# Kernel tuning notes

Hardware: AMD Instinct MI355X
Metric: run time of the kernel (lower is better)

## Reference

```python
import jax, jax.numpy as jnp
import numpy as np

N = 40000   # query points
M = 40000   # support points
H = 32      # neighbors per query
CIN = 64
COUT = 64
KS = 3      # kernel points per dim
PDIM = 3
K = KS ** PDIM  # 27 kernel points
RADIUS = 1.0
KP_EXTENT = RADIUS / (KS - 1) * PDIM ** 0.5


def _kernel_points():
    # replicates KPConv.getKernelPoints: grid of KS^PDIM points in a ball of RADIUS
    xyz = np.linspace(-1.0, 1.0, KS)
    pts = np.meshgrid(*PDIM * [xyz])
    pts = np.vstack([p.flatten() for p in pts]).T  # [K, PDIM]
    pts = pts / PDIM ** 0.5
    return (pts * RADIUS).astype(np.float32)


def setup_inputs() -> dict:
    key = jax.random.key(0)
    k1, k2, k3, k4, k5 = jax.random.split(key, 5)
    q_pts = jax.random.uniform(k1, (N, PDIM), dtype=jnp.float32) * 10.0
    s_pts = jax.random.uniform(k2, (M, PDIM), dtype=jnp.float32) * 10.0
    neighb_inds = jax.random.randint(k3, (N, H), 0, M + 1)  # M == shadow index
    x = jax.random.normal(k4, (M, CIN), dtype=jnp.float32)
    # kaiming-uniform-like init for weights [K, CIN, COUT]
    bound = (6.0 / ((1.0 + 5.0) * CIN)) ** 0.5
    weights = jax.random.uniform(k5, (K, CIN, COUT), dtype=jnp.float32,
                                 minval=-bound, maxval=bound)
    kernel_points = jnp.asarray(_kernel_points())
    return {"q_pts": q_pts, "s_pts": s_pts, "neighb_inds": neighb_inds,
            "x": x, "weights": weights, "kernel_points": kernel_points}


def reference(q_pts, s_pts, neighb_inds, x, weights, kernel_points):
    # append shadow support point (far away) and zero shadow feature
    s_pts_p = jnp.concatenate(
        [s_pts, jnp.full((1, s_pts.shape[-1]), 1e6, dtype=s_pts.dtype)], axis=0)
    x_p = jnp.concatenate(
        [x, jnp.zeros((1, x.shape[-1]), dtype=x.dtype)], axis=0)

    neighbors = s_pts_p[neighb_inds] - q_pts[:, None, :]        # [N, H, 3]
    neighb_x = x_p[neighb_inds]                                  # [N, H, CIN]

    # distance of each neighbor to each kernel point
    diff = neighbors[:, :, None, :] - kernel_points              # [N, H, K, 3]
    sq_d = jnp.sum(diff * diff, axis=-1)                         # [N, H, K]
    all_w = jnp.clip(1.0 - jnp.sqrt(sq_d) / KP_EXTENT, 0.0)      # [N, H, K]

    # all_weights^T @ neighb_x  -> [N, K, CIN]
    weighted = jnp.einsum('nhk,nhc->nkc', all_w, neighb_x)
    # per-kernel-point matmul with weights [K, CIN, COUT], summed over K
    out = jnp.einsum('nkc,kco->no', weighted, weights)           # [N, COUT]
    return out
```

## Files before the change

### kernel.cpp

```cpp
#include <hip/hip_runtime.h>

typedef short bf16x8 __attribute__((ext_vector_type(8)));
typedef float f32x4  __attribute__((ext_vector_type(4)));

#define HN    32
#define CIN   64
#define KP    27
#define QB    64
#define CAPB  96
#define NTB   1024
#define OSTR  65

#define QB2   32
#define CAP2  64
#define OSTR2 68

#define INV_EXT 1.1547005383792517f
#define CUT2    3.4821f

__device__ __forceinline__ unsigned f2bf(float f){
    union{float fv;unsigned u;}v; v.fv=f;
    unsigned u=v.u;
    u += 0x7fffu + ((u>>16)&1u);
    return u>>16;
}

__global__ void pack_spts(const float* __restrict__ s, float4* __restrict__ o, int M){
    int i = blockIdx.x*256 + threadIdx.x;
    if (i < M) o[i] = make_float4(s[i*3+0], s[i*3+1], s[i*3+2], 0.f);
}

__global__ void pack_wt2(const float* __restrict__ W, unsigned short* __restrict__ Wt2){
    int tid = blockIdx.x*256 + threadIdx.x;
    if (tid >= KP*8*64) return;
    int lane = tid & 63;
    int f  = (tid>>6) & 7;
    int k  = tid >> 9;
    int ot = f>>1, ks = f&1, g = lane>>4;
    unsigned r[8];
#pragma unroll
    for (int j=0;j<8;++j)
        r[j] = f2bf(W[(size_t)k*4096 + (size_t)(ks*32 + g*8 + j)*64 + ot*16 + (lane&15)]);
    uint4 v; v.x=r[0]|(r[1]<<16); v.y=r[2]|(r[3]<<16); v.z=r[4]|(r[5]<<16); v.w=r[6]|(r[7]<<16);
    *(uint4*)&Wt2[(size_t)tid*8] = v;
}

__global__ __launch_bounds__(256)
void kp_prep2(const float* __restrict__ s, const float* __restrict__ W,
              float4* __restrict__ o, unsigned short* __restrict__ Wt2, int M)
{
    int tid = blockIdx.x*256 + threadIdx.x;
    if (tid < M) o[tid] = make_float4(s[tid*3+0], s[tid*3+1], s[tid*3+2], 0.f);
    if (tid < KP*8*64){
        int lane = tid & 63;
        int f  = (tid>>6) & 7;
        int kk = tid >> 9;
        int ot = f>>1, ks = f&1, gg = lane>>4;
        unsigned r[8];
#pragma unroll
        for (int j=0;j<8;++j)
            r[j] = f2bf(W[(size_t)kk*4096 + (size_t)(ks*32 + gg*8 + j)*64 + ot*16 + (lane&15)]);
        uint4 v; v.x=r[0]|(r[1]<<16); v.y=r[2]|(r[3]<<16); v.z=r[4]|(r[5]<<16); v.w=r[6]|(r[7]<<16);
        *(uint4*)&Wt2[(size_t)tid*8] = v;
    }
}

__device__ __forceinline__ void loadB(const unsigned short* __restrict__ Wt2, int k, int lane,
                                      bf16x8 (&b)[8]){
    const unsigned short* base = Wt2 + ((size_t)(k*8)*64 + lane)*8;
#pragma unroll
    for (int f=0;f<8;++f) b[f] = *(const bf16x8*)(base + f*512);
}
__device__ __forceinline__ bf16x8 ldBf(const unsigned short* __restrict__ Wt2, int k, int f, int lane){
    return *(const bf16x8*)(Wt2 + ((size_t)(k*8 + f)*64 + lane)*8);
}
__device__ __forceinline__ void loadB_w(const float* __restrict__ W, int k, int lane, int g,
                                        bf16x8 (&b)[8]){
#pragma unroll
    for (int f=0;f<8;++f){
        int ot=f>>1, ks=f&1;
        union{unsigned u[4]; bf16x8 v;} bb;
#pragma unroll
        for (int jj=0;jj<4;++jj){
            unsigned l0=f2bf(W[(size_t)k*4096 + (size_t)(ks*32+g*8+2*jj)*64   + ot*16+(lane&15)]);
            unsigned l1=f2bf(W[(size_t)k*4096 + (size_t)(ks*32+g*8+2*jj+1)*64 + ot*16+(lane&15)]);
            bb.u[jj]=l0|(l1<<16);
        }
        b[f]=bb.v;
    }
}

__global__ __launch_bounds__(256,5)
void kpconv_fused(const float* __restrict__ q_pts, const int* __restrict__ inds,
                  const float* __restrict__ x, const float* __restrict__ kpts,
                  const float4* __restrict__ sp4, const unsigned short* __restrict__ Wt2,
                  float* __restrict__ out, int N, int M)
{
    __shared__ unsigned short rows[64*CIN];
    __shared__ __align__(16) float wlds[KP*64];
    __shared__ __align__(16) float outacc[QB2*OSTR2];
    __shared__ float qls[QB2*3];
    __shared__ float bx[CAP2], by[CAP2], bz[CAP2];
    __shared__ __align__(16) int bq[CAP2];
    __shared__ int bixs[CAP2];
    __shared__ int cnt;

    const int t    = threadIdx.x;
    const int lane = t & 63;
    const int wv   = t >> 6;
    const int g    = lane >> 4;
    const int r15  = lane & 15;
    const int nq0  = blockIdx.x * QB2;
    const int NP   = N*HN;

    for (int j=t; j<QB2*OSTR2; j+=256) outacc[j]=0.f;
    for (int j=t; j<QB2*3;    j+=256){ int gi=nq0*3+j; qls[j]=(gi<N*3)? q_pts[gi]:0.f; }
    if (t < CAP2) bq[t]=0;
    if (t==0) cnt=0;
    __syncthreads();

#pragma unroll
    for (int jj=0; jj<4; ++jj){
        int pl   = jj*256 + t;
        int pair = nq0*HN + pl;
        if (pair < NP){
            int idx = inds[pair];
            if ((unsigned)idx < (unsigned)M){
                int q = pl >> 5;
                float4 s4 = sp4[idx];
                float px=s4.x-qls[q*3], py=s4.y-qls[q*3+1], pz=s4.z-qls[q*3+2];
                if (px*px+py*py+pz*pz <= CUT2){
                    int sl = atomicAdd(&cnt, 1);
                    if (sl < CAP2){ bx[sl]=px; by[sl]=py; bz[sl]=pz; bq[sl]=q; bixs[sl]=idx; }
                }
            }
        }
    }
    __syncthreads();
    const int total = cnt;

    auto processTile = [&](int cc){
        const int nrow = (cc + 15) & ~15;
        const int f0 = wv*2, f1 = wv*2+1;
        bf16x8 Bc0 = ldBf(Wt2, 0, f0, lane);
        bf16x8 Bc1 = ldBf(Wt2, 0, f1, lane);
        for (int it=t; it<nrow*8; it+=256){
            int rl=it>>3, c8=it&7;
            uint4 v; v.x=0u; v.y=0u; v.z=0u; v.w=0u;
            if (rl < cc){
                int ix = bixs[rl];
                const float4* xr = (const float4*)(x + (size_t)ix*CIN);
                float4 fr0=xr[c8*2], fr1=xr[c8*2+1];
                v.x=f2bf(fr0.x)|(f2bf(fr0.y)<<16); v.y=f2bf(fr0.z)|(f2bf(fr0.w)<<16);
                v.z=f2bf(fr1.x)|(f2bf(fr1.y)<<16); v.w=f2bf(fr1.z)|(f2bf(fr1.w)<<16);
            }
            int ba = rl*128 + ((c8*16)^((rl&7)<<4));
            *(uint4*)((char*)rows+ba) = v;
        }
        for (int i=t; i<KP*64; i+=256){
            int row = i&63;
            if (row >= nrow) continue;
            int k = i>>6;
            float w=0.f;
            if (row < cc){
                float dx=bx[row]-kpts[k*3+0];
                float dy=by[row]-kpts[k*3+1];
                float dz=bz[row]-kpts[k*3+2];
                w = fmaxf(1.f - sqrtf(dx*dx+dy*dy+dz*dz)*INV_EXT, 0.f);
            }
            wlds[i]=w;
        }
        __syncthreads();

        const char* rb = (const char*)rows;
        bf16x8 A0[4], A1[4];
#pragma unroll
        for (int rt=0; rt<4; ++rt){
            if (rt*16 >= cc) continue;
            int row = rt*16 + r15;
            A0[rt] = *(const bf16x8*)(rb + row*128 + (( g*16)    ^((row&7)<<4)));
            A1[rt] = *(const bf16x8*)(rb + row*128 + ((64+g*16)  ^((row&7)<<4)));
        }
        f32x4 acc[4];
#pragma unroll
        for (int rt=0; rt<4; ++rt){ acc[rt][0]=0.f; acc[rt][1]=0.f; acc[rt][2]=0.f; acc[rt][3]=0.f; }

#pragma unroll 1
        for (int k=0; k<KP; ++k){
            int kn = (k+1 < KP) ? (k+1) : k;
            bf16x8 Bn0 = ldBf(Wt2, kn, f0, lane);
            bf16x8 Bn1 = ldBf(Wt2, kn, f1, lane);
            const float* wk = &wlds[k*64];
#pragma unroll
            for (int rt=0; rt<4; ++rt){
                if (rt*16 >= cc) continue;
                f32x4 w4 = *(const f32x4*)(wk + rt*16 + g*4);
                bool act = (w4[0]>0.f)|(w4[1]>0.f)|(w4[2]>0.f)|(w4[3]>0.f);
                if (__any(act)){
                    f32x4 c; c[0]=0.f; c[1]=0.f; c[2]=0.f; c[3]=0.f;
                    c = __builtin_amdgcn_mfma_f32_16x16x32_bf16(A0[rt], Bc0, c, 0,0,0);
                    c = __builtin_amdgcn_mfma_f32_16x16x32_bf16(A1[rt], Bc1, c, 0,0,0);
                    acc[rt][0] += w4[0]*c[0];
                    acc[rt][1] += w4[1]*c[1];
                    acc[rt][2] += w4[2]*c[2];
                    acc[rt][3] += w4[3]*c[3];
                }
            }
            Bc0 = Bn0; Bc1 = Bn1;
        }
#pragma unroll
        for (int rt=0; rt<4; ++rt){
            if (rt*16 >= cc) continue;
            int4 q4 = *(const int4*)&bq[rt*16 + g*4];
#pragma unroll
            for (int rr=0; rr<4; ++rr){
                float val = acc[rt][rr];
                int qv = (rr==0)? q4.x : (rr==1)? q4.y : (rr==2)? q4.z : q4.w;
                if (val != 0.f)
                    atomicAdd(&outacc[qv*OSTR2 + wv*16 + r15], val);
            }
        }
        __syncthreads();
    };

    if (total <= CAP2){
        if (total > 0) processTile(total);
    } else {
        for (int w=0; w<(QB2*HN)/64; ++w){
            __syncthreads();
            if (t==0) cnt=0;
            __syncthreads();
            if (t < 64){
                int pl = w*64 + t, pair = nq0*HN + pl;
                if (pair < NP){
                    int idx = inds[pair];
                    if ((unsigned)idx < (unsigned)M){
                        int q = pl >> 5;
                        float4 s4 = sp4[idx];
                        float px=s4.x-qls[q*3], py=s4.y-qls[q*3+1], pz=s4.z-qls[q*3+2];
                        if (px*px+py*py+pz*pz <= CUT2){
                            int sl = atomicAdd(&cnt, 1);
                            bx[sl]=px; by[sl]=py; bz[sl]=pz; bq[sl]=q; bixs[sl]=idx;
                        }
                    }
                }
            }
            __syncthreads();
            if (cnt > 0) processTile(cnt);
        }
    }
    __syncthreads();

    for (int j=t; j<QB2*16; j+=256){
        int q=j>>4, o4=j&15, n=nq0+q;
        if (n < N)
            ((float4*)out)[(size_t)n*16 + o4] = *(const float4*)&outacc[q*OSTR2 + o4*4];
    }
}


__global__ __launch_bounds__(NTB)
void kpconv6(const float* __restrict__ q_pts, const float* __restrict__ s_pts,
             const int* __restrict__ inds, const float* __restrict__ x,
             const float* __restrict__ W, const float* __restrict__ kpts,
             const float4* __restrict__ sp4, const unsigned short* __restrict__ Wt2,
             int use_ws, float* __restrict__ out, int N, int M)
{
    __shared__ float qls[QB*3];
    __shared__ float posx[CAPB], posy[CAPB], posz[CAPB];
    __shared__ int   eqb[CAPB], eidxb[CAPB];
    __shared__ unsigned short rows[CAPB*CIN];
    __shared__ float outacc[QB*OSTR];
    __shared__ int   cnt;

    const int t    = threadIdx.x;
    const int lane = t & 63;
    const int wv   = t >> 6;
    const int g    = lane >> 4;
    const int r15  = lane & 15;
    const int nq0  = blockIdx.x * QB;

    const int k0 = wv, k1 = wv + 16;
    const bool has2 = (k1 < KP);

    bf16x8 B0[8], B1[8];
    if (use_ws){
        loadB(Wt2, k0, lane, B0);
        loadB(Wt2, has2 ? k1 : k0, lane, B1);
    } else {
        loadB_w(W, k0, lane, g, B0);
        loadB_w(W, has2 ? k1 : k0, lane, g, B1);
    }
    const float k0x=kpts[k0*3+0], k0y=kpts[k0*3+1], k0z=kpts[k0*3+2];
    float k1x=0.f,k1y=0.f,k1z=0.f;
    if (has2){ k1x=kpts[k1*3+0]; k1y=kpts[k1*3+1]; k1z=kpts[k1*3+2]; }

    for (int j=t; j<QB*OSTR; j+=NTB) outacc[j]=0.f;
    for (int j=t; j<QB*3;   j+=NTB){ int gi=nq0*3+j; qls[j]=(gi<N*3)? q_pts[gi]:0.f; }
    if (t==0) cnt=0;
    __syncthreads();

    auto process = [&](int cc){
        if (cc<=0) return;
        const int ntile=(cc+15)>>4, nrow=ntile*16;
        for (int j=cc+t; j<nrow; j+=NTB){ posx[j]=1e9f; posy[j]=1e9f; posz[j]=1e9f; eqb[j]=0; }
        for (int it=t; it<nrow*8; it+=NTB){
            int e=it>>3, c8=it&7;
            uint4 v; v.x=0u; v.y=0u; v.z=0u; v.w=0u;
            if (e<cc){
                const float4* xr=(const float4*)(x+(size_t)eidxb[e]*CIN);
                float4 f0=xr[c8*2], f1=xr[c8*2+1];
                v.x=f2bf(f0.x)|(f2bf(f0.y)<<16); v.y=f2bf(f0.z)|(f2bf(f0.w)<<16);
                v.z=f2bf(f1.x)|(f2bf(f1.y)<<16); v.w=f2bf(f1.z)|(f2bf(f1.w)<<16);
            }
            int ba=e*128+((c8*16)^((e&7)<<4));
            *(uint4*)((char*)rows+ba)=v;
        }
        __syncthreads();
        for (int tile=0; tile<ntile; ++tile){
            const char* rb=(const char*)rows;
            int row=tile*16+r15;
            bf16x8 a0=*(const bf16x8*)(rb+row*128+((g*16)    ^((row&7)<<4)));
            bf16x8 a1=*(const bf16x8*)(rb+row*128+((64+g*16) ^((row&7)<<4)));
            int rbase=tile*16+g*4;
            float w0[4], w1[4]; int qq[4];
#pragma unroll
            for (int r=0;r<4;++r){
                float sx=posx[rbase+r], sy=posy[rbase+r], sz=posz[rbase+r];
                qq[r]=eqb[rbase+r];
                float dx=sx-k0x, dy=sy-k0y, dz=sz-k0z;
                w0[r]=fmaxf(1.f-sqrtf(dx*dx+dy*dy+dz*dz)*INV_EXT,0.f);
                float ex=sx-k1x, ey=sy-k1y, ez=sz-k1z;
                float w1r=fmaxf(1.f-sqrtf(ex*ex+ey*ey+ez*ez)*INV_EXT,0.f);
                w1[r]=has2? w1r : 0.f;
            }
#pragma unroll
            for (int ot=0;ot<4;++ot){
                f32x4 c={0.f,0.f,0.f,0.f};
                c=__builtin_amdgcn_mfma_f32_16x16x32_bf16(a0,B0[2*ot],c,0,0,0);
                c=__builtin_amdgcn_mfma_f32_16x16x32_bf16(a1,B0[2*ot+1],c,0,0,0);
                f32x4 d={0.f,0.f,0.f,0.f};
                if (has2){
                    d=__builtin_amdgcn_mfma_f32_16x16x32_bf16(a0,B1[2*ot],d,0,0,0);
                    d=__builtin_amdgcn_mfma_f32_16x16x32_bf16(a1,B1[2*ot+1],d,0,0,0);
                }
#pragma unroll
                for (int r=0;r<4;++r){
                    float val=w0[r]*c[r]+w1[r]*d[r];
                    if (val!=0.f) atomicAdd(&outacc[qq[r]*OSTR+ot*16+r15], val);
                }
            }
        }
        __syncthreads();
    };

    for (int it=t; it<QB*HN; it+=NTB){
        int q=it>>5, h=it&31, n=nq0+q;
        bool inr=false; int idx=0; float px=0.f,py=0.f,pz=0.f;
        if (n<N){
            idx=inds[(size_t)n*HN+h];
            if ((unsigned)idx<(unsigned)M){
                float sx,sy,sz;
                if (use_ws){ float4 s4=sp4[idx]; sx=s4.x; sy=s4.y; sz=s4.z; }
                else { sx=s_pts[idx*3]; sy=s_pts[idx*3+1]; sz=s_pts[idx*3+2]; }
                px=sx-qls[q*3]; py=sy-qls[q*3+1]; pz=sz-qls[q*3+2];
                inr=(px*px+py*py+pz*pz)<=CUT2;
            }
        }
        if (inr){
            int sl=atomicAdd(&cnt,1);
            if (sl<CAPB){ eqb[sl]=q; eidxb[sl]=idx; posx[sl]=px; posy[sl]=py; posz[sl]=pz; }
        }
    }
    __syncthreads();
    const int total=cnt;

    if (total<=CAPB){
        process(total);
    } else {
        for (int w=0; w<(QB*HN)/64; ++w){
            __syncthreads();
            if (t==0) cnt=0;
            __syncthreads();
            if (t<64){
                int pair=w*64+t;
                int q=pair>>5, h=pair&31, n=nq0+q;
                if (n<N){
                    int idx=inds[(size_t)n*HN+h];
                    if ((unsigned)idx<(unsigned)M){
                        float sx,sy,sz;
                        if (use_ws){ float4 s4=sp4[idx]; sx=s4.x; sy=s4.y; sz=s4.z; }
                        else { sx=s_pts[idx*3]; sy=s_pts[idx*3+1]; sz=s_pts[idx*3+2]; }
                        float px=sx-qls[q*3], py=sy-qls[q*3+1], pz=sz-qls[q*3+2];
                        if (px*px+py*py+pz*pz<=CUT2){
                            int sl=atomicAdd(&cnt,1);
                            eqb[sl]=q; eidxb[sl]=idx; posx[sl]=px; posy[sl]=py; posz[sl]=pz;
                        }
                    }
                }
            }
            __syncthreads();
            process(cnt);
        }
    }
    __syncthreads();

    for (int j=t; j<QB*CIN; j+=NTB){
        int q=j>>6, o=j&63, n=nq0+q;
        if (n<N) out[(size_t)n*CIN+o]=outacc[q*OSTR+o];
    }
}

extern "C" void kernel_launch(void* const* d_in, const int* in_sizes, int n_in,
                              void* d_out, int out_size, void* d_ws, size_t ws_size,
                              hipStream_t stream)
{
    const float* q_pts=(const float*)d_in[0];
    const float* s_pts=(const float*)d_in[1];
    const int*   inds =(const int*)d_in[2];
    const float* x    =(const float*)d_in[3];
    const float* W    =(const float*)d_in[4];
    const float* kpts =(const float*)d_in[5];
    float* outp=(float*)d_out;
    int N=in_sizes[0]/3;
    int M=in_sizes[1]/3;

    char* wsb=(char*)d_ws;
    float4* sp4=(float4*)wsb;
    unsigned short* Wt2=(unsigned short*)(wsb + (size_t)M*16);

    const size_t WT2B = (size_t)KP*8*64*8*2;
    size_t need = (size_t)M*16 + WT2B;

    if (ws_size >= need){
        int prepN = (M > KP*8*64) ? M : KP*8*64;
        hipLaunchKernelGGL(kp_prep2, dim3((prepN+255)/256), dim3(256), 0, stream,
                           s_pts, W, sp4, Wt2, M);
        int nblocks = (N + QB2 - 1) / QB2;
        hipLaunchKernelGGL(kpconv_fused, dim3(nblocks), dim3(256), 0, stream,
                           q_pts, inds, x, kpts, sp4, Wt2, outp, N, M);
        return;
    }

    hipLaunchKernelGGL(kpconv6, dim3((N+QB-1)/QB), dim3(NTB), 0, stream,
                       q_pts, s_pts, inds, x, W, kpts, sp4, Wt2, 0, outp, N, M);
}
```

Measured before the change: 41.34 us.

## Split kernel points across waves instead of output tiles in fused KPConv

The fused kernel changes its work split. Before, each wave owned one 16-column output tile and looped over all 27 kernel points. Now each wave owns a strided subset of kernel points, loads all 8 B fragments per kernel point, and computes all four output tiles over 32-row chunks. The neighbor index and support-point loads are batched ahead of the filtering, and the feature-row gathers are issued before the weight computation so their latency overlaps. Launch bounds drop occupancy from 5 to 4 blocks per CU to make room for the larger accumulator and B register sets. This also raises atomic traffic into shared-memory outacc, because each wave now contributes partial sums for every output column. Dead pack kernels and the use_ws path in the fallback kernel are removed.

New measurement: 51.43 us. 1.24x slower.

```diff
diff --git a/kernel.cpp b/kernel.cpp
--- a/kernel.cpp
+++ b/kernel.cpp
@@ -23,26 +23,6 @@
     unsigned u=v.u;
     u += 0x7fffu + ((u>>16)&1u);
     return u>>16;
-}
-
-__global__ void pack_spts(const float* __restrict__ s, float4* __restrict__ o, int M){
-    int i = blockIdx.x*256 + threadIdx.x;
-    if (i < M) o[i] = make_float4(s[i*3+0], s[i*3+1], s[i*3+2], 0.f);
-}
-
-__global__ void pack_wt2(const float* __restrict__ W, unsigned short* __restrict__ Wt2){
-    int tid = blockIdx.x*256 + threadIdx.x;
-    if (tid >= KP*8*64) return;
-    int lane = tid & 63;
-    int f  = (tid>>6) & 7;
-    int k  = tid >> 9;
-    int ot = f>>1, ks = f&1, g = lane>>4;
-    unsigned r[8];
-#pragma unroll
-    for (int j=0;j<8;++j)
-        r[j] = f2bf(W[(size_t)k*4096 + (size_t)(ks*32 + g*8 + j)*64 + ot*16 + (lane&15)]);
-    uint4 v; v.x=r[0]|(r[1]<<16); v.y=r[2]|(r[3]<<16); v.z=r[4]|(r[5]<<16); v.w=r[6]|(r[7]<<16);
-    *(uint4*)&Wt2[(size_t)tid*8] = v;
 }
 
 __global__ __launch_bounds__(256)
@@ -71,9 +51,6 @@
 #pragma unroll
     for (int f=0;f<8;++f) b[f] = *(const bf16x8*)(base + f*512);
 }
-__device__ __forceinline__ bf16x8 ldBf(const unsigned short* __restrict__ Wt2, int k, int f, int lane){
-    return *(const bf16x8*)(Wt2 + ((size_t)(k*8 + f)*64 + lane)*8);
-}
 __device__ __forceinline__ void loadB_w(const float* __restrict__ W, int k, int lane, int g,
                                         bf16x8 (&b)[8]){
 #pragma unroll
@@ -90,7 +67,7 @@
     }
 }
 
-__global__ __launch_bounds__(256,5)
+__global__ __launch_bounds__(256,4)
 void kpconv_fused(const float* __restrict__ q_pts, const int* __restrict__ inds,
                   const float* __restrict__ x, const float* __restrict__ kpts,
                   const float4* __restrict__ sp4, const unsigned short* __restrict__ Wt2,
@@ -101,8 +78,7 @@
     __shared__ __align__(16) float outacc[QB2*OSTR2];
     __shared__ float qls[QB2*3];
     __shared__ float bx[CAP2], by[CAP2], bz[CAP2];
-    __shared__ __align__(16) int bq[CAP2];
-    __shared__ int bixs[CAP2];
+    __shared__ int bq[CAP2], bixs[CAP2];
     __shared__ int cnt;
 
     const int t    = threadIdx.x;
@@ -119,44 +95,44 @@
     if (t==0) cnt=0;
     __syncthreads();
 
+    int idxv[4];
 #pragma unroll
     for (int jj=0; jj<4; ++jj){
-        int pl   = jj*256 + t;
-        int pair = nq0*HN + pl;
-        if (pair < NP){
-            int idx = inds[pair];
-            if ((unsigned)idx < (unsigned)M){
-                int q = pl >> 5;
-                float4 s4 = sp4[idx];
-                float px=s4.x-qls[q*3], py=s4.y-qls[q*3+1], pz=s4.z-qls[q*3+2];
-                if (px*px+py*py+pz*pz <= CUT2){
-                    int sl = atomicAdd(&cnt, 1);
-                    if (sl < CAP2){ bx[sl]=px; by[sl]=py; bz[sl]=pz; bq[sl]=q; bixs[sl]=idx; }
-                }
+        int pair = nq0*HN + jj*256 + t;
+        idxv[jj] = (pair < NP) ? inds[pair] : M;
+    }
+    float4 s4v[4];
+#pragma unroll
+    for (int jj=0; jj<4; ++jj){
+        int ic = (idxv[jj] < M) ? idxv[jj] : 0;
+        s4v[jj] = sp4[ic];
+    }
+#pragma unroll
+    for (int jj=0; jj<4; ++jj){
+        if (idxv[jj] < M){
+            int q = (jj*256 + t) >> 5;
+            float px=s4v[jj].x-qls[q*3], py=s4v[jj].y-qls[q*3+1], pz=s4v[jj].z-qls[q*3+2];
+            if (px*px+py*py+pz*pz <= CUT2){
+                int sl = atomicAdd(&cnt, 1);
+                if (sl < CAP2){ bx[sl]=px; by[sl]=py; bz[sl]=pz; bq[sl]=q; bixs[sl]=idxv[jj]; }
             }
         }
     }
     __syncthreads();
     const int total = cnt;
 
-    auto processTile = [&](int cc){
+    auto process = [&](int cc){
         const int nrow = (cc + 15) & ~15;
-        const int f0 = wv*2, f1 = wv*2+1;
-        bf16x8 Bc0 = ldBf(Wt2, 0, f0, lane);
-        bf16x8 Bc1 = ldBf(Wt2, 0, f1, lane);
-        for (int it=t; it<nrow*8; it+=256){
-            int rl=it>>3, c8=it&7;
-            uint4 v; v.x=0u; v.y=0u; v.z=0u; v.w=0u;
-            if (rl < cc){
-                int ix = bixs[rl];
-                const float4* xr = (const float4*)(x + (size_t)ix*CIN);
-                float4 fr0=xr[c8*2], fr1=xr[c8*2+1];
-                v.x=f2bf(fr0.x)|(f2bf(fr0.y)<<16); v.y=f2bf(fr0.z)|(f2bf(fr0.w)<<16);
-                v.z=f2bf(fr1.x)|(f2bf(fr1.y)<<16); v.w=f2bf(fr1.z)|(f2bf(fr1.w)<<16);
-            }
-            int ba = rl*128 + ((c8*16)^((rl&7)<<4));
-            *(uint4*)((char*)rows+ba) = v;
-        }
+        int itA=t, itB=t+256;
+        int rlA=itA>>3, c8A=itA&7, rlB=itB>>3, c8B=itB&7;
+        bool vA=(rlA<cc), vB=(rlB<cc);
+        bool wrA=(rlA<nrow), wrB=(rlB<nrow);
+        int ixA = vA ? bixs[rlA] : bixs[0];
+        int ixB = vB ? bixs[rlB] : bixs[0];
+        const float4* xrA = (const float4*)(x + (size_t)ixA*CIN);
+        const float4* xrB = (const float4*)(x + (size_t)ixB*CIN);
+        float4 fA0=xrA[c8A*2], fA1=xrA[c8A*2+1];
+        float4 fB0=xrB[c8B*2], fB1=xrB[c8B*2+1];
         for (int i=t; i<KP*64; i+=256){
             int row = i&63;
             if (row >= nrow) continue;
@@ -170,61 +146,97 @@
             }
             wlds[i]=w;
         }
+        if (wrA){
+            uint4 v; v.x=0u; v.y=0u; v.z=0u; v.w=0u;
+            if (vA){
+                v.x=f2bf(fA0.x)|(f2bf(fA0.y)<<16); v.y=f2bf(fA0.z)|(f2bf(fA0.w)<<16);
+                v.z=f2bf(fA1.x)|(f2bf(fA1.y)<<16); v.w=f2bf(fA1.z)|(f2bf(fA1.w)<<16);
+            }
+            *(uint4*)((char*)rows + rlA*128 + ((c8A*16)^((rlA&7)<<4))) = v;
+        }
+        if (wrB){
+            uint4 v; v.x=0u; v.y=0u; v.z=0u; v.w=0u;
+            if (vB){
+                v.x=f2bf(fB0.x)|(f2bf(fB0.y)<<16); v.y=f2bf(fB0.z)|(f2bf(fB0.w)<<16);
+                v.z=f2bf(fB1.x)|(f2bf(fB1.y)<<16); v.w=f2bf(fB1.z)|(f2bf(fB1.w)<<16);
+            }
+            *(uint4*)((char*)rows + rlB*128 + ((c8B*16)^((rlB&7)<<4))) = v;
+        }
         __syncthreads();
 
         const char* rb = (const char*)rows;
-        bf16x8 A0[4], A1[4];
-#pragma unroll
-        for (int rt=0; rt<4; ++rt){
-            if (rt*16 >= cc) continue;
-            int row = rt*16 + r15;
-            A0[rt] = *(const bf16x8*)(rb + row*128 + (( g*16)    ^((row&7)<<4)));
-            A1[rt] = *(const bf16x8*)(rb + row*128 + ((64+g*16)  ^((row&7)<<4)));
-        }
-        f32x4 acc[4];
-#pragma unroll
-        for (int rt=0; rt<4; ++rt){ acc[rt][0]=0.f; acc[rt][1]=0.f; acc[rt][2]=0.f; acc[rt][3]=0.f; }
+        for (int ch=0; ch*32 < cc; ++ch){
+            bool rtv[2];
+            bf16x8 A0[2], A1[2];
+#pragma unroll
+            for (int rt=0; rt<2; ++rt){
+                rtv[rt] = (ch*32 + rt*16) < cc;
+                int row = ch*32 + rt*16 + r15;
+                int rc  = rtv[rt] ? row : r15;
+                A0[rt] = *(const bf16x8*)(rb + rc*128 + (( g*16)   ^((rc&7)<<4)));
+                A1[rt] = *(const bf16x8*)(rb + rc*128 + ((64+g*16) ^((rc&7)<<4)));
+            }
+            f32x4 acc[2][4];
+#pragma unroll
+            for (int rt=0; rt<2; ++rt)
+#pragma unroll
+                for (int ot=0; ot<4; ++ot){ f32x4 z={0.f,0.f,0.f,0.f}; acc[rt][ot]=z; }
 
 #pragma unroll 1
-        for (int k=0; k<KP; ++k){
-            int kn = (k+1 < KP) ? (k+1) : k;
-            bf16x8 Bn0 = ldBf(Wt2, kn, f0, lane);
-            bf16x8 Bn1 = ldBf(Wt2, kn, f1, lane);
-            const float* wk = &wlds[k*64];
-#pragma unroll
-            for (int rt=0; rt<4; ++rt){
-                if (rt*16 >= cc) continue;
-                f32x4 w4 = *(const f32x4*)(wk + rt*16 + g*4);
-                bool act = (w4[0]>0.f)|(w4[1]>0.f)|(w4[2]>0.f)|(w4[3]>0.f);
-                if (__any(act)){
-                    f32x4 c; c[0]=0.f; c[1]=0.f; c[2]=0.f; c[3]=0.f;
-                    c = __builtin_amdgcn_mfma_f32_16x16x32_bf16(A0[rt], Bc0, c, 0,0,0);
-                    c = __builtin_amdgcn_mfma_f32_16x16x32_bf16(A1[rt], Bc1, c, 0,0,0);
-                    acc[rt][0] += w4[0]*c[0];
-                    acc[rt][1] += w4[1]*c[1];
-                    acc[rt][2] += w4[2]*c[2];
-                    acc[rt][3] += w4[3]*c[3];
-                }
-            }
-            Bc0 = Bn0; Bc1 = Bn1;
-        }
-#pragma unroll
-        for (int rt=0; rt<4; ++rt){
-            if (rt*16 >= cc) continue;
-            int4 q4 = *(const int4*)&bq[rt*16 + g*4];
-#pragma unroll
-            for (int rr=0; rr<4; ++rr){
-                float val = acc[rt][rr];
-                int qv = (rr==0)? q4.x : (rr==1)? q4.y : (rr==2)? q4.z : q4.w;
-                if (val != 0.f)
-                    atomicAdd(&outacc[qv*OSTR2 + wv*16 + r15], val);
+            for (int j=0; j<7; ++j){
+                int k = wv + 4*j;
+                bool hask = (k < KP);
+                int kl = hask ? k : 0;
+                bf16x8 B[8];
+                loadB(Wt2, kl, lane, B);
+                const float* wk = &wlds[kl*64 + ch*32];
+                f32x4 w4[2];
+#pragma unroll
+                for (int rt=0; rt<2; ++rt){
+                    f32x4 z={0.f,0.f,0.f,0.f};
+                    if (rtv[rt]) z = *(const f32x4*)(wk + rt*16 + g*4);
+                    w4[rt]=z;
+                }
+                if (!hask) continue;
+#pragma unroll
+                for (int rt=0; rt<2; ++rt){
+                    bool act = rtv[rt] && __any(w4[rt][0]>0.f || w4[rt][1]>0.f ||
+                                                w4[rt][2]>0.f || w4[rt][3]>0.f);
+                    if (act){
+#pragma unroll
+                        for (int ot=0; ot<4; ++ot){
+                            f32x4 c={0.f,0.f,0.f,0.f};
+                            c = __builtin_amdgcn_mfma_f32_16x16x32_bf16(A0[rt], B[2*ot  ], c, 0,0,0);
+                            c = __builtin_amdgcn_mfma_f32_16x16x32_bf16(A1[rt], B[2*ot+1], c, 0,0,0);
+                            acc[rt][ot][0] += w4[rt][0]*c[0];
+                            acc[rt][ot][1] += w4[rt][1]*c[1];
+                            acc[rt][ot][2] += w4[rt][2]*c[2];
+                            acc[rt][ot][3] += w4[rt][3]*c[3];
+                        }
+                    }
+                }
+            }
+#pragma unroll
+            for (int rt=0; rt<2; ++rt){
+                if (!rtv[rt]) continue;
+                int rbase = ch*32 + rt*16 + g*4;
+#pragma unroll
+                for (int rr=0; rr<4; ++rr){
+                    int qv = bq[rbase+rr];
+#pragma unroll
+                    for (int ot=0; ot<4; ++ot){
+                        float val = acc[rt][ot][rr];
+                        if (val != 0.f)
+                            atomicAdd(&outacc[qv*OSTR2 + ot*16 + r15], val);
+                    }
+                }
             }
         }
         __syncthreads();
     };
 
     if (total <= CAP2){
-        if (total > 0) processTile(total);
+        if (total > 0) process(total);
     } else {
         for (int w=0; w<(QB2*HN)/64; ++w){
             __syncthreads();
@@ -246,7 +258,7 @@
                 }
             }
             __syncthreads();
-            if (cnt > 0) processTile(cnt);
+            if (cnt > 0) process(cnt);
         }
     }
     __syncthreads();
@@ -263,8 +275,7 @@
 void kpconv6(const float* __restrict__ q_pts, const float* __restrict__ s_pts,
              const int* __restrict__ inds, const float* __restrict__ x,
              const float* __restrict__ W, const float* __restrict__ kpts,
-             const float4* __restrict__ sp4, const unsigned short* __restrict__ Wt2,
-             int use_ws, float* __restrict__ out, int N, int M)
+             float* __restrict__ out, int N, int M)
 {
     __shared__ float qls[QB*3];
     __shared__ float posx[CAPB], posy[CAPB], posz[CAPB];
@@ -284,13 +295,8 @@
     const bool has2 = (k1 < KP);
 
     bf16x8 B0[8], B1[8];
-    if (use_ws){
-        loadB(Wt2, k0, lane, B0);
-        loadB(Wt2, has2 ? k1 : k0, lane, B1);
-    } else {
-        loadB_w(W, k0, lane, g, B0);
-        loadB_w(W, has2 ? k1 : k0, lane, g, B1);
-    }
+    loadB_w(W, k0, lane, g, B0);
+    loadB_w(W, has2 ? k1 : k0, lane, g, B1);
     const float k0x=kpts[k0*3+0], k0y=kpts[k0*3+1], k0z=kpts[k0*3+2];
     float k1x=0.f,k1y=0.f,k1z=0.f;
     if (has2){ k1x=kpts[k1*3+0]; k1y=kpts[k1*3+1]; k1z=kpts[k1*3+2]; }
@@ -360,9 +366,7 @@
         if (n<N){
             idx=inds[(size_t)n*HN+h];
             if ((unsigned)idx<(unsigned)M){
-                float sx,sy,sz;
-                if (use_ws){ float4 s4=sp4[idx]; sx=s4.x; sy=s4.y; sz=s4.z; }
-                else { sx=s_pts[idx*3]; sy=s_pts[idx*3+1]; sz=s_pts[idx*3+2]; }
+                float sx=s_pts[idx*3], sy=s_pts[idx*3+1], sz=s_pts[idx*3+2];
                 px=sx-qls[q*3]; py=sy-qls[q*3+1]; pz=sz-qls[q*3+2];
                 inr=(px*px+py*py+pz*pz)<=CUT2;
             }
@@ -388,9 +392,7 @@
                 if (n<N){
                     int idx=inds[(size_t)n*HN+h];
                     if ((unsigned)idx<(unsigned)M){
-                        float sx,sy,sz;
-                        if (use_ws){ float4 s4=sp4[idx]; sx=s4.x; sy=s4.y; sz=s4.z; }
-                        else { sx=s_pts[idx*3]; sy=s_pts[idx*3+1]; sz=s_pts[idx*3+2]; }
+                        float sx=s_pts[idx*3], sy=s_pts[idx*3+1], sz=s_pts[idx*3+2];
                         float px=sx-qls[q*3], py=sy-qls[q*3+1], pz=sz-qls[q*3+2];
                         if (px*px+py*py+pz*pz<=CUT2){
                             int sl=atomicAdd(&cnt,1);
@@ -443,5 +445,5 @@
     }
 
     hipLaunchKernelGGL(kpconv6, dim3((N+QB-1)/QB), dim3(NTB), 0, stream,
-                       q_pts, s_pts, inds, x, W, kpts, sp4, Wt2, 0, outp, N, M);
-}
+                       q_pts, s_pts, inds, x, W, kpts, outp, N, M);
+}
```
